# Performance work log

Measured on AMD Instinct MI355X. Metric: run time of the kernel, lower is better.

Reference implementation:

```python
import jax, jax.numpy as jnp
import numpy as np

B, H, S, D = 4, 16, 2048, 128

def setup_inputs() -> dict:
    key = jax.random.key(0)
    kq, kk, kv = jax.random.split(key, 3)
    q = jax.random.normal(kq, (B, H, S, D), dtype=jnp.float32)
    k = jax.random.normal(kk, (B, H, S, D), dtype=jnp.float32)
    v = jax.random.normal(kv, (B, H, S, D), dtype=jnp.float32)
    # causal mask: True = masked (upper triangle above the diagonal)
    mask = jnp.triu(jnp.ones((S, S), dtype=jnp.bool_), k=1)[None, None, :, :]
    return {"q": q, "k": k, "v": v, "mask": mask}

def reference(q, k, v, mask):
    head_dim = q.shape[-1]
    scale = 1.0 / jnp.sqrt(jnp.float32(head_dim))
    # scores: [B, H, Sq, Sk]
    scores = jnp.einsum('bhqd,bhkd->bhqk', q, k) * scale
    scores = jnp.where(mask, -jnp.inf, scores)
    attention_weights = jax.nn.softmax(scores, axis=-1)
    # dropout p=0.0 (eval): identity
    context_vectors = jnp.einsum('bhqk,bhkd->bhqd', attention_weights, v)
    return (context_vectors, attention_weights)
```

## Files before the change

kernel.cpp:

```cpp
#include <hip/hip_runtime.h>
#include <hip/hip_bf16.h>

#define S_LEN 2048
#define D_DIM 128
#define BH_N  64
#define BC    64
#define SCALE 0.08838834764831845f
#define SD    (S_LEN * D_DIM)
#define WS_NEED ((size_t)BH_N * SD * 2)

typedef __attribute__((ext_vector_type(8)))  short short8;
typedef __attribute__((ext_vector_type(16))) float f32x16;
typedef __attribute__((ext_vector_type(4)))  float fv4;

__device__ __forceinline__ ushort f2bf(float f) {
  union { float f; unsigned u; } x; x.f = f;
  unsigned r = x.u + 0x7FFFu + ((x.u >> 16) & 1u);
  return (ushort)(r >> 16);
}

__device__ __forceinline__ short8 pack8(float4 a, float4 b) {
  short8 p;
  p[0] = (short)f2bf(a.x); p[1] = (short)f2bf(a.y);
  p[2] = (short)f2bf(a.z); p[3] = (short)f2bf(a.w);
  p[4] = (short)f2bf(b.x); p[5] = (short)f2bf(b.y);
  p[6] = (short)f2bf(b.z); p[7] = (short)f2bf(b.w);
  return p;
}

__global__ __launch_bounds__(256) void cvt_k_kernel(
    const float* __restrict__ k, ushort* __restrict__ kb) {
  size_t total = (size_t)BH_N * SD / 8;
  for (size_t i = (size_t)blockIdx.x * 256 + threadIdx.x; i < total;
       i += (size_t)gridDim.x * 256) {
    float4 a = *(const float4*)(k + i * 8);
    float4 b = *(const float4*)(k + i * 8 + 4);
    *(short8*)(kb + i * 8) = pack8(a, b);
  }
}

template <bool KB16>
__device__ __forceinline__ void do_A(
    int bh, int qb,
    const float* __restrict__ q, const float* __restrict__ k,
    const ushort* __restrict__ kb, const float* __restrict__ v,
    float* __restrict__ ctx,
    char* klds, char* vtlds, char* plds, float (*lred)[64]) {
  const int tid  = threadIdx.x;
  const int lane = tid & 63;
  const int w    = tid >> 6;
  const int wq   = w >> 1, wk = w & 1;
  const int l31  = lane & 31, lhi = lane >> 5;

  const float*  qbase  = q  + (size_t)bh * SD;
  const float*  kbase  = k  + (size_t)bh * SD;
  const ushort* kbbase = kb + (size_t)bh * SD;
  const float*  vbase  = v  + (size_t)bh * SD;

  short8 qf[8];
  {
    const float* qrow = qbase + (size_t)(qb * 64 + wq * 32 + l31) * D_DIM;
    #pragma unroll
    for (int s = 0; s < 8; ++s) {
      int d0 = 16 * s + 8 * lhi;
      float4 a = *(const float4*)(qrow + d0);
      float4 b = *(const float4*)(qrow + d0 + 4);
      qf[s] = pack8(a, b);
    }
  }

  float4 kreg[8], vreg[8];
  short8 kreg16[4];

  auto load_k = [&](int kt) {
    int trow = tid >> 2, tc = tid & 3;
    if constexpr (KB16) {
      const ushort* src = kbbase + (size_t)(kt * BC + trow) * D_DIM;
      #pragma unroll
      for (int i = 0; i < 4; ++i)
        kreg16[i] = *(const short8*)(src + tc * 8 + i * 32);
    } else {
      const float* src = kbase + (size_t)(kt * BC + trow) * D_DIM;
      #pragma unroll
      for (int i = 0; i < 4; ++i) {
        int c0 = tc * 8 + i * 32;
        kreg[2 * i]     = *(const float4*)(src + c0);
        kreg[2 * i + 1] = *(const float4*)(src + c0 + 4);
      }
    }
  };
  auto write_k = [&]() {
    int trow = tid >> 2, tc = tid & 3;
    #pragma unroll
    for (int i = 0; i < 4; ++i) {
      int c0 = tc * 8 + i * 32;
      int off = (trow * 256 + c0 * 2) ^ ((trow & 7) << 4);
      if constexpr (KB16)
        *(short8*)(klds + off) = kreg16[i];
      else
        *(short8*)(klds + off) = pack8(kreg[2 * i], kreg[2 * i + 1]);
    }
  };
  auto load_v = [&](int kt) {
    int kp = tid & 31, dg = tid >> 5;
    const float* r0 = vbase + (size_t)(kt * BC + 2 * kp) * D_DIM + dg * 16;
    #pragma unroll
    for (int i = 0; i < 4; ++i) {
      vreg[i]     = *(const float4*)(r0 + 4 * i);
      vreg[4 + i] = *(const float4*)(r0 + D_DIM + 4 * i);
    }
  };
  auto write_v = [&]() {
    int kp = tid & 31, dg = tid >> 5;
    #pragma unroll
    for (int j = 0; j < 16; ++j) {
      int d = dg * 16 + j;
      float lo = vreg[j >> 2][j & 3];
      float hi = vreg[4 + (j >> 2)][j & 3];
      unsigned u = (unsigned)f2bf(lo) | ((unsigned)f2bf(hi) << 16);
      int off = (d * 128 + kp * 4) ^ ((d & 7) << 4);
      *(unsigned*)(vtlds + off) = u;
    }
  };

  auto compute_s = [&]() -> f32x16 {
    f32x16 acc;
    #pragma unroll
    for (int i = 0; i < 16; ++i) acc[i] = 0.f;
    int krow = wk * 32 + l31;
    int base = krow * 256;
    int swz  = (krow & 7) << 4;
    #pragma unroll
    for (int s = 0; s < 8; ++s) {
      int off = (base + 32 * s + 16 * lhi) ^ swz;
      short8 kf = *(const short8*)(klds + off);
      acc = __builtin_amdgcn_mfma_f32_32x32x16_bf16(qf[s], kf, acc, 0, 0, 0);
    }
    return acc;
  };

  float l_lane[16];
  f32x16 o0, o1;
  #pragma unroll
  for (int i = 0; i < 16; ++i) { l_lane[i] = 0.f; o0[i] = 0.f; o1[i] = 0.f; }

  load_k(0); load_v(0);

  for (int kt = 0; kt <= qb; ++kt) {
    write_k(); write_v();
    if (kt < qb) { load_k(kt + 1); load_v(kt + 1); }
    __syncthreads();

    f32x16 acc = compute_s();
    int kcol_l = wk * 32 + l31;
    int kcol = kt * BC + kcol_l;
    bool diag = (kt == qb);
    #pragma unroll
    for (int r = 0; r < 16; ++r) {
      int rl = wq * 32 + (r & 3) + 8 * (r >> 2) + 4 * lhi;
      int qrow = qb * 64 + rl;
      float e = (diag && kcol > qrow) ? 0.f : __expf(acc[r] * SCALE);
      l_lane[r] += e;
      int poff = (rl * 128 + kcol_l * 2) ^ ((rl & 7) << 4);
      *(ushort*)(plds + poff) = f2bf(e);
    }
    __syncthreads();

    #pragma unroll
    for (int s = 0; s < 4; ++s) {
      int prow = wq * 32 + l31;
      int paoff = (prow * 128 + (16 * s + 8 * lhi) * 2) ^ ((prow & 7) << 4);
      short8 pa = *(const short8*)(plds + paoff);
      int kko = (16 * s + 8 * lhi) * 2;
      int d0 = wk * 64 + l31;
      int d1 = d0 + 32;
      int off0 = (d0 * 128 + kko) ^ ((d0 & 7) << 4);
      int off1 = (d1 * 128 + kko) ^ ((d1 & 7) << 4);
      short8 vb0 = *(const short8*)(vtlds + off0);
      short8 vb1 = *(const short8*)(vtlds + off1);
      o0 = __builtin_amdgcn_mfma_f32_32x32x16_bf16(pa, vb0, o0, 0, 0, 0);
      o1 = __builtin_amdgcn_mfma_f32_32x32x16_bf16(pa, vb1, o1, 0, 0, 0);
    }
    __syncthreads();
  }

  #pragma unroll
  for (int r = 0; r < 16; ++r) {
    float x = l_lane[r];
    x += __shfl_xor(x, 1);  x += __shfl_xor(x, 2);  x += __shfl_xor(x, 4);
    x += __shfl_xor(x, 8);  x += __shfl_xor(x, 16);
    l_lane[r] = x;
  }
  if (l31 == 0) {
    #pragma unroll
    for (int r = 0; r < 16; ++r) {
      int rl = wq * 32 + (r & 3) + 8 * (r >> 2) + 4 * lhi;
      lred[wk][rl] = l_lane[r];
    }
  }
  __syncthreads();

  float inv_l[16];
  #pragma unroll
  for (int r = 0; r < 16; ++r) {
    int rl = wq * 32 + (r & 3) + 8 * (r >> 2) + 4 * lhi;
    inv_l[r] = 1.0f / (lred[0][rl] + lred[1][rl]);
  }
  #pragma unroll
  for (int r = 0; r < 16; ++r) {
    int rl = wq * 32 + (r & 3) + 8 * (r >> 2) + 4 * lhi;
    size_t obase = (size_t)(bh * S_LEN + qb * 64 + rl) * D_DIM;
    ctx[obase + wk * 64 + l31]      = o0[r] * inv_l[r];
    ctx[obase + wk * 64 + 32 + l31] = o1[r] * inv_l[r];
  }
}

template <bool KB16>
__device__ __forceinline__ void do_B2(
    int bh, int panel,
    const float* __restrict__ q, const float* __restrict__ k,
    const ushort* __restrict__ kb, float* __restrict__ wts) {
  const int tid  = threadIdx.x;
  const int lane = tid & 63;
  const int w    = tid >> 6;
  const int l31  = lane & 31, lhi = lane >> 5;

  const int qrow0 = panel * 128 + w * 32;
  float* wbase = wts + ((size_t)bh * S_LEN + qrow0) * S_LEN;

  short8 qf[8];
  {
    const float* qrow = q + ((size_t)bh * S_LEN + qrow0 + l31) * D_DIM;
    #pragma unroll
    for (int s = 0; s < 8; ++s) {
      int d0 = 16 * s + 8 * lhi;
      float4 a = *(const float4*)(qrow + d0);
      float4 b = *(const float4*)(qrow + d0 + 4);
      qf[s] = pack8(a, b);
    }
  }

  const int qmax = qrow0 + 31;
  const ushort* kbb = kb + (size_t)bh * SD;
  const float*  kfb = k  + (size_t)bh * SD;

  float l_lane[16];
  #pragma unroll
  for (int r = 0; r < 16; ++r) l_lane[r] = 0.f;

  const int nkt = qmax / 64 + 1;
  for (int kt = 0; kt < nkt; ++kt) {
    f32x16 a0, a1;
    #pragma unroll
    for (int i = 0; i < 16; ++i) { a0[i] = 0.f; a1[i] = 0.f; }
    if constexpr (KB16) {
      const ushort* k0 = kbb + (size_t)(kt * 64 + l31) * D_DIM;
      const ushort* k1 = k0 + 32 * D_DIM;
      #pragma unroll
      for (int s8 = 0; s8 < 8; ++s8) {
        int d0 = 16 * s8 + 8 * lhi;
        short8 kf0 = *(const short8*)(k0 + d0);
        short8 kf1 = *(const short8*)(k1 + d0);
        a0 = __builtin_amdgcn_mfma_f32_32x32x16_bf16(qf[s8], kf0, a0, 0, 0, 0);
        a1 = __builtin_amdgcn_mfma_f32_32x32x16_bf16(qf[s8], kf1, a1, 0, 0, 0);
      }
    } else {
      const float* k0 = kfb + (size_t)(kt * 64 + l31) * D_DIM;
      const float* k1 = k0 + 32 * D_DIM;
      #pragma unroll
      for (int s8 = 0; s8 < 8; ++s8) {
        int d0 = 16 * s8 + 8 * lhi;
        short8 kf0 = pack8(*(const float4*)(k0 + d0), *(const float4*)(k0 + d0 + 4));
        short8 kf1 = pack8(*(const float4*)(k1 + d0), *(const float4*)(k1 + d0 + 4));
        a0 = __builtin_amdgcn_mfma_f32_32x32x16_bf16(qf[s8], kf0, a0, 0, 0, 0);
        a1 = __builtin_amdgcn_mfma_f32_32x32x16_bf16(qf[s8], kf1, a1, 0, 0, 0);
      }
    }
    const int kc0 = kt * 64 + l31, kc1 = kc0 + 32;
    #pragma unroll
    for (int r = 0; r < 16; ++r) {
      int qr = qrow0 + (r & 3) + 8 * (r >> 2) + 4 * lhi;
      float e0 = (kc0 > qr) ? 0.f : __expf(a0[r] * SCALE);
      float e1 = (kc1 > qr) ? 0.f : __expf(a1[r] * SCALE);
      l_lane[r] += e0 + e1;
    }
  }

  float invl[16];
  #pragma unroll
  for (int r = 0; r < 16; ++r) {
    float x = l_lane[r];
    x += __shfl_xor(x, 1);  x += __shfl_xor(x, 2);  x += __shfl_xor(x, 4);
    x += __shfl_xor(x, 8);  x += __shfl_xor(x, 16);
    invl[r] = 1.0f / x;
  }

  const int nkg = qmax / 256 + 1;
  for (int kg = 0; kg < nkg; ++kg) {
    f32x16 ac[8];
    #pragma unroll
    for (int t = 0; t < 8; ++t)
      #pragma unroll
      for (int i = 0; i < 16; ++i) ac[t][i] = 0.f;

    #pragma unroll
    for (int t = 0; t < 4; ++t) {
      const int tc0 = kg * 256 + t * 64;
      if (tc0 <= qmax) {
        if constexpr (KB16) {
          const ushort* k0 = kbb + (size_t)(tc0 + l31) * D_DIM;
          const ushort* k1 = k0 + 32 * D_DIM;
          #pragma unroll
          for (int s8 = 0; s8 < 8; ++s8) {
            int d0 = 16 * s8 + 8 * lhi;
            short8 kf0 = *(const short8*)(k0 + d0);
            short8 kf1 = *(const short8*)(k1 + d0);
            ac[2 * t]     = __builtin_amdgcn_mfma_f32_32x32x16_bf16(qf[s8], kf0, ac[2 * t], 0, 0, 0);
            ac[2 * t + 1] = __builtin_amdgcn_mfma_f32_32x32x16_bf16(qf[s8], kf1, ac[2 * t + 1], 0, 0, 0);
          }
        } else {
          const float* k0 = kfb + (size_t)(tc0 + l31) * D_DIM;
          const float* k1 = k0 + 32 * D_DIM;
          #pragma unroll
          for (int s8 = 0; s8 < 8; ++s8) {
            int d0 = 16 * s8 + 8 * lhi;
            short8 kf0 = pack8(*(const float4*)(k0 + d0), *(const float4*)(k0 + d0 + 4));
            short8 kf1 = pack8(*(const float4*)(k1 + d0), *(const float4*)(k1 + d0 + 4));
            ac[2 * t]     = __builtin_amdgcn_mfma_f32_32x32x16_bf16(qf[s8], kf0, ac[2 * t], 0, 0, 0);
            ac[2 * t + 1] = __builtin_amdgcn_mfma_f32_32x32x16_bf16(qf[s8], kf1, ac[2 * t + 1], 0, 0, 0);
          }
        }
      }
    }

    #pragma unroll
    for (int t = 0; t < 4; ++t) {
      const int kc0 = kg * 256 + t * 64 + l31;
      const int kc1 = kc0 + 32;
      #pragma unroll
      for (int r = 0; r < 16; ++r) {
        int qr = qrow0 + (r & 3) + 8 * (r >> 2) + 4 * lhi;
        ac[2 * t][r]     = (kc0 > qr) ? 0.f : __expf(ac[2 * t][r] * SCALE) * invl[r];
        ac[2 * t + 1][r] = (kc1 > qr) ? 0.f : __expf(ac[2 * t + 1][r] * SCALE) * invl[r];
      }
    }

    float* gbase = wbase + kg * 256 + lane;
    #pragma unroll
    for (int r = 0; r < 16; ++r) {
      int rA = (r & 3) + 8 * (r >> 2);
      float* rpA = gbase + (size_t)rA * S_LEN;
      float* rpB = gbase + (size_t)(rA + 4) * S_LEN;
      #pragma unroll
      for (int t = 0; t < 4; ++t) {
        float sA = __shfl(ac[2 * t + 1][r], lane ^ 32);
        float vA = lhi ? sA : ac[2 * t][r];
        __builtin_nontemporal_store(vA, rpA + t * 64);
      }
      #pragma unroll
      for (int t = 0; t < 4; ++t) {
        float sB = __shfl(ac[2 * t][r], lane ^ 32);
        float vB = lhi ? ac[2 * t + 1][r] : sB;
        __builtin_nontemporal_store(vB, rpB + t * 64);
      }
    }
  }

  fv4 z = (fv4)0.f;
  const int c0 = nkg * 256;
  for (int rr = 0; rr < 32; ++rr) {
    float* rowp = wbase + (size_t)rr * S_LEN;
    for (int c = c0 + lane * 4; c < S_LEN; c += 256)
      __builtin_nontemporal_store(z, (fv4*)(rowp + c));
  }
}

template <bool KB16>
__global__ __launch_bounds__(256, 2) void attn_combo_kernel(
    const float* __restrict__ q, const float* __restrict__ k,
    const ushort* __restrict__ kb, const float* __restrict__ v,
    float* __restrict__ ctx, float* __restrict__ wts) {
  __shared__ __align__(16) char klds[BC * 256];
  __shared__ __align__(16) char vtlds[D_DIM * 128];
  __shared__ __align__(16) char plds[64 * 128];
  __shared__ float lred[2][64];

  const int bid = blockIdx.x;
  const int xcd = bid & 7;
  const int seq = bid >> 3;
  const int m   = seq % 3;

  if (m < 2) {
    int a_idx = (seq / 3) * 2 + m;
    int bh    = xcd + 8 * (a_idx & 7);
    int qb    = 31 - (a_idx >> 3);
    do_A<KB16>(bh, qb, q, k, kb, v, ctx, klds, vtlds, plds, lred);
  } else {
    int b_idx = seq / 3;
    int bh    = xcd + 8 * (b_idx & 7);
    int panel = 15 - (b_idx >> 3);
    do_B2<KB16>(bh, panel, q, k, kb, wts);
  }
}

extern "C" void kernel_launch(void* const* d_in, const int* in_sizes, int n_in,
                              void* d_out, int out_size, void* d_ws, size_t ws_size,
                              hipStream_t stream) {
  const float* q = (const float*)d_in[0];
  const float* k = (const float*)d_in[1];
  const float* v = (const float*)d_in[2];
  float* ctx = (float*)d_out;
  float* wts = ctx + (size_t)BH_N * SD;
  ushort* kb16 = (ushort*)d_ws;

  if (ws_size >= WS_NEED) {
    cvt_k_kernel<<<dim3(2048), dim3(256), 0, stream>>>(k, kb16);
    attn_combo_kernel<true><<<dim3(3072), dim3(256), 0, stream>>>(
        q, k, kb16, v, ctx, wts);
  } else {
    attn_combo_kernel<false><<<dim3(3072), dim3(256), 0, stream>>>(
        q, k, kb16, v, ctx, wts);
  }
}
```

Baseline: 550.0 us.

## Dump unnormalized bf16 probabilities in flash pass, normalize weights in relay kernel

Adds a flash-style attention kernel that computes the softmax numerators once, writes them as compact bf16 triangle tiles to the workspace along with the row sums, and finishes the context. A second kernel reads these tiles, scales them by the inverse row sum and writes the full fp32 weight matrix, zero-filling the masked region. This replaces the earlier combo kernel, which recomputed QK^T in a separate weights pass, with one compute pass plus a streaming relay. It needs a much larger workspace, and the exponentials are taken without max subtraction, so very large scores could overflow.

Measured after the change: 571.1 us. 3.8% more time.

```diff
diff --git a/kernel.cpp b/kernel.cpp
--- a/kernel.cpp
+++ b/kernel.cpp
@@ -5,11 +5,20 @@
 #define D_DIM 128
 #define BH_N  64
 #define BC    64
+#define NTILE 32
 #define SCALE 0.08838834764831845f
 #define SD    (S_LEN * D_DIM)
-#define WS_NEED ((size_t)BH_N * SD * 2)
+
+#define LSUM_BYTES (BH_N * S_LEN * 4)
+#define KB16_OFF   ((size_t)LSUM_BYTES)
+#define KB16_BYTES ((size_t)BH_N * SD * 2)
+#define P_OFF      (KB16_OFF + KB16_BYTES)
+#define P_HEAD     ((size_t)8192 * 528)
+#define WS_FULL    (P_OFF + (size_t)BH_N * P_HEAD)
+#define WS_KB16    (KB16_OFF + KB16_BYTES)
 
 typedef __attribute__((ext_vector_type(8)))  short short8;
+typedef __attribute__((ext_vector_type(4)))  short short4v;
 typedef __attribute__((ext_vector_type(16))) float f32x16;
 typedef __attribute__((ext_vector_type(4)))  float fv4;
 
@@ -17,6 +26,9 @@
   union { float f; unsigned u; } x; x.f = f;
   unsigned r = x.u + 0x7FFFu + ((x.u >> 16) & 1u);
   return (ushort)(r >> 16);
+}
+__device__ __forceinline__ float bf2f(ushort u) {
+  union { unsigned i; float f; } x; x.i = (unsigned)u << 16; return x.f;
 }
 
 __device__ __forceinline__ short8 pack8(float4 a, float4 b) {
@@ -26,6 +38,13 @@
   p[4] = (short)f2bf(b.x); p[5] = (short)f2bf(b.y);
   p[6] = (short)f2bf(b.z); p[7] = (short)f2bf(b.w);
   return p;
+}
+
+__device__ __forceinline__ void map_block_a(int bid, int& bh, int& qb) {
+  int xcd  = bid & 7;
+  int rest = bid >> 3;
+  bh = (rest >> 5) * 8 + xcd;
+  qb = (NTILE - 1) - (rest & 31);
 }
 
 __global__ __launch_bounds__(256) void cvt_k_kernel(
@@ -36,6 +55,224 @@
     float4 a = *(const float4*)(k + i * 8);
     float4 b = *(const float4*)(k + i * 8 + 4);
     *(short8*)(kb + i * 8) = pack8(a, b);
+  }
+}
+
+__global__ __launch_bounds__(256, 2) void attn_flash_dump_kernel(
+    const float* __restrict__ q, const ushort* __restrict__ kb,
+    const float* __restrict__ v, float* __restrict__ ctx,
+    float* __restrict__ lsum_out, char* __restrict__ pws) {
+  __shared__ __align__(16) char klds[BC * 256];
+  __shared__ __align__(16) char vtlds[D_DIM * 128];
+  __shared__ __align__(16) char plds[64 * 128];
+  __shared__ float lred[2][64];
+
+  const int tid  = threadIdx.x;
+  const int lane = tid & 63;
+  const int w    = tid >> 6;
+  const int wq   = w >> 1, wk = w & 1;
+  const int l31  = lane & 31, lhi = lane >> 5;
+
+  int bh, qb;
+  map_block_a(blockIdx.x, bh, qb);
+
+  const float*  qbase  = q  + (size_t)bh * SD;
+  const ushort* kbbase = kb + (size_t)bh * SD;
+  const float*  vbase  = v  + (size_t)bh * SD;
+  char* pdump = pws + (size_t)bh * P_HEAD + (size_t)8192 * (qb * (qb + 1) / 2);
+  const size_t prow_bytes = (size_t)(qb + 1) * 128;
+
+  short8 qf[8];
+  {
+    const float* qrow = qbase + (size_t)(qb * 64 + wq * 32 + l31) * D_DIM;
+    #pragma unroll
+    for (int s = 0; s < 8; ++s) {
+      int d0 = 16 * s + 8 * lhi;
+      float4 a = *(const float4*)(qrow + d0);
+      float4 b = *(const float4*)(qrow + d0 + 4);
+      qf[s] = pack8(a, b);
+    }
+  }
+
+  float4 vreg[8];
+  short8 kreg16[4];
+
+  auto load_k = [&](int kt) {
+    int trow = tid >> 2, tc = tid & 3;
+    const ushort* src = kbbase + (size_t)(kt * BC + trow) * D_DIM;
+    #pragma unroll
+    for (int i = 0; i < 4; ++i)
+      kreg16[i] = *(const short8*)(src + tc * 8 + i * 32);
+  };
+  auto write_k = [&]() {
+    int trow = tid >> 2, tc = tid & 3;
+    #pragma unroll
+    for (int i = 0; i < 4; ++i) {
+      int c0 = tc * 8 + i * 32;
+      int off = (trow * 256 + c0 * 2) ^ ((trow & 7) << 4);
+      *(short8*)(klds + off) = kreg16[i];
+    }
+  };
+  auto load_v = [&](int kt) {
+    int kp = tid & 31, dg = tid >> 5;
+    const float* r0 = vbase + (size_t)(kt * BC + 2 * kp) * D_DIM + dg * 16;
+    #pragma unroll
+    for (int i = 0; i < 4; ++i) {
+      vreg[i]     = *(const float4*)(r0 + 4 * i);
+      vreg[4 + i] = *(const float4*)(r0 + D_DIM + 4 * i);
+    }
+  };
+  auto write_v = [&]() {
+    int kp = tid & 31, dg = tid >> 5;
+    #pragma unroll
+    for (int j = 0; j < 16; ++j) {
+      int d = dg * 16 + j;
+      float lo = vreg[j >> 2][j & 3];
+      float hi = vreg[4 + (j >> 2)][j & 3];
+      unsigned u = (unsigned)f2bf(lo) | ((unsigned)f2bf(hi) << 16);
+      int off = (d * 128 + kp * 4) ^ ((d & 7) << 4);
+      *(unsigned*)(vtlds + off) = u;
+    }
+  };
+
+  auto compute_s = [&]() -> f32x16 {
+    f32x16 acc;
+    #pragma unroll
+    for (int i = 0; i < 16; ++i) acc[i] = 0.f;
+    int krow = wk * 32 + l31;
+    int base = krow * 256;
+    int swz  = (krow & 7) << 4;
+    #pragma unroll
+    for (int s = 0; s < 8; ++s) {
+      int off = (base + 32 * s + 16 * lhi) ^ swz;
+      short8 kf = *(const short8*)(klds + off);
+      acc = __builtin_amdgcn_mfma_f32_32x32x16_bf16(qf[s], kf, acc, 0, 0, 0);
+    }
+    return acc;
+  };
+
+  float l_lane[16];
+  f32x16 o0, o1;
+  #pragma unroll
+  for (int i = 0; i < 16; ++i) { l_lane[i] = 0.f; o0[i] = 0.f; o1[i] = 0.f; }
+
+  load_k(0); load_v(0);
+
+  for (int kt = 0; kt <= qb; ++kt) {
+    write_k(); write_v();
+    if (kt < qb) { load_k(kt + 1); load_v(kt + 1); }
+    __syncthreads();
+
+    f32x16 acc = compute_s();
+    int kcol_l = wk * 32 + l31;
+    int kcol = kt * BC + kcol_l;
+    bool diag = (kt == qb);
+    #pragma unroll
+    for (int r = 0; r < 16; ++r) {
+      int rl = wq * 32 + (r & 3) + 8 * (r >> 2) + 4 * lhi;
+      int qrow = qb * 64 + rl;
+      float e = (diag && kcol > qrow) ? 0.f : __expf(acc[r] * SCALE);
+      l_lane[r] += e;
+      int poff = (rl * 128 + kcol_l * 2) ^ ((rl & 7) << 4);
+      *(ushort*)(plds + poff) = f2bf(e);
+    }
+    __syncthreads();
+
+    #pragma unroll
+    for (int s = 0; s < 4; ++s) {
+      int prow = wq * 32 + l31;
+      int paoff = (prow * 128 + (16 * s + 8 * lhi) * 2) ^ ((prow & 7) << 4);
+      short8 pa = *(const short8*)(plds + paoff);
+      int kko = (16 * s + 8 * lhi) * 2;
+      int d0 = wk * 64 + l31;
+      int d1 = d0 + 32;
+      int off0 = (d0 * 128 + kko) ^ ((d0 & 7) << 4);
+      int off1 = (d1 * 128 + kko) ^ ((d1 & 7) << 4);
+      short8 vb0 = *(const short8*)(vtlds + off0);
+      short8 vb1 = *(const short8*)(vtlds + off1);
+      o0 = __builtin_amdgcn_mfma_f32_32x32x16_bf16(pa, vb0, o0, 0, 0, 0);
+      o1 = __builtin_amdgcn_mfma_f32_32x32x16_bf16(pa, vb1, o1, 0, 0, 0);
+    }
+
+    {
+      const int row = tid >> 2;
+      const int c32 = (tid & 3) * 32;
+      const int swzr = (row & 7) << 4;
+      short8 lo = *(const short8*)(plds + ((row * 128 + c32) ^ swzr));
+      short8 hi = *(const short8*)(plds + ((row * 128 + c32 + 16) ^ swzr));
+      char* dst = pdump + (size_t)row * prow_bytes + (size_t)kt * 128 + c32;
+      __builtin_nontemporal_store(lo, (short8*)dst);
+      __builtin_nontemporal_store(hi, (short8*)(dst + 16));
+    }
+    __syncthreads();
+  }
+
+  #pragma unroll
+  for (int r = 0; r < 16; ++r) {
+    float x = l_lane[r];
+    x += __shfl_xor(x, 1);  x += __shfl_xor(x, 2);  x += __shfl_xor(x, 4);
+    x += __shfl_xor(x, 8);  x += __shfl_xor(x, 16);
+    l_lane[r] = x;
+  }
+  if (l31 == 0) {
+    #pragma unroll
+    for (int r = 0; r < 16; ++r) {
+      int rl = wq * 32 + (r & 3) + 8 * (r >> 2) + 4 * lhi;
+      lred[wk][rl] = l_lane[r];
+    }
+  }
+  __syncthreads();
+
+  if (tid < 64)
+    lsum_out[(size_t)bh * S_LEN + qb * 64 + tid] = lred[0][tid] + lred[1][tid];
+
+  float inv_l[16];
+  #pragma unroll
+  for (int r = 0; r < 16; ++r) {
+    int rl = wq * 32 + (r & 3) + 8 * (r >> 2) + 4 * lhi;
+    inv_l[r] = 1.0f / (lred[0][rl] + lred[1][rl]);
+  }
+  #pragma unroll
+  for (int r = 0; r < 16; ++r) {
+    int rl = wq * 32 + (r & 3) + 8 * (r >> 2) + 4 * lhi;
+    size_t obase = (size_t)(bh * S_LEN + qb * 64 + rl) * D_DIM;
+    ctx[obase + wk * 64 + l31]      = o0[r] * inv_l[r];
+    ctx[obase + wk * 64 + 32 + l31] = o1[r] * inv_l[r];
+  }
+}
+
+__global__ __launch_bounds__(256) void attn_wts_relay_kernel(
+    const ushort* __restrict__ pws, const float* __restrict__ lsum,
+    float* __restrict__ wts) {
+  int bh, qb;
+  map_block_a(blockIdx.x, bh, qb);
+  const int tid  = threadIdx.x;
+  const int lane = tid & 63;
+  const int w    = tid >> 6;
+
+  const ushort* pbase =
+      pws + (size_t)bh * (P_HEAD / 2) + (size_t)4096 * (qb * (qb + 1) / 2);
+  const int Wcols = (qb + 1) * 64;
+  float* wtile = wts + ((size_t)(bh * S_LEN + qb * 64)) * S_LEN;
+
+  for (int i = 0; i < 16; ++i) {
+    int row = i * 4 + w;
+    float invl = 1.0f / lsum[(size_t)bh * S_LEN + qb * 64 + row];
+    const ushort* pr = pbase + (size_t)row * Wcols;
+    float* out = wtile + (size_t)row * S_LEN;
+    #pragma unroll
+    for (int ch = 0; ch < 8; ++ch) {
+      int col = ch * 256 + lane * 4;
+      fv4 val = (fv4)0.f;
+      if (col < Wcols) {
+        short4v p = *(const short4v*)(pr + col);
+        val[0] = bf2f((ushort)p[0]) * invl;
+        val[1] = bf2f((ushort)p[1]) * invl;
+        val[2] = bf2f((ushort)p[2]) * invl;
+        val[3] = bf2f((ushort)p[3]) * invl;
+      }
+      *(fv4*)(out + col) = val;
+    }
   }
 }
 
@@ -411,9 +648,18 @@
   const float* v = (const float*)d_in[2];
   float* ctx = (float*)d_out;
   float* wts = ctx + (size_t)BH_N * SD;
-  ushort* kb16 = (ushort*)d_ws;
-
-  if (ws_size >= WS_NEED) {
+
+  float*  lsum = (float*)d_ws;
+  ushort* kb16 = (ushort*)((char*)d_ws + KB16_OFF);
+  char*   pws  = (char*)d_ws + P_OFF;
+
+  if (ws_size >= WS_FULL) {
+    cvt_k_kernel<<<dim3(2048), dim3(256), 0, stream>>>(k, kb16);
+    attn_flash_dump_kernel<<<dim3(BH_N * NTILE), dim3(256), 0, stream>>>(
+        q, kb16, v, ctx, lsum, pws);
+    attn_wts_relay_kernel<<<dim3(BH_N * NTILE), dim3(256), 0, stream>>>(
+        (const ushort*)pws, lsum, wts);
+  } else if (ws_size >= WS_KB16) {
     cvt_k_kernel<<<dim3(2048), dim3(256), 0, stream>>>(k, kb16);
     attn_combo_kernel<true><<<dim3(3072), dim3(256), 0, stream>>>(
         q, k, kb16, v, ctx, wts);
```
